# Kernel optimization log

Measured on AMD Instinct MI355X. Metric: run time of the kernel, lower is better.

Reference implementation:

```python
import jax, jax.numpy as jnp
import numpy as np

N_QUBITS = 6
N_LAYERS = 2
DIM = 2 ** N_QUBITS  # 64


def _apply_1q(state, U, q):
    """Apply a 1-qubit gate U on qubit q. state: (B, 2,...,2); U: (2,2) or (B,2,2)."""
    s = jnp.moveaxis(state, 1 + q, -1)
    if U.ndim == 3:  # batched gate (angle embedding)
        s = jnp.einsum('bij,b...j->b...i', U, s)
    else:
        s = jnp.einsum('ij,...j->...i', U, s)
    return jnp.moveaxis(s, -1, 1 + q)


def _cnot(state, c, t):
    """CNOT with control qubit c, target qubit t on (B, 2,...,2) state."""
    ax_c = 1 + c
    s0 = jax.lax.index_in_dim(state, 0, ax_c, keepdims=False)
    s1 = jax.lax.index_in_dim(state, 1, ax_c, keepdims=False)
    ax_t = 1 + t if t < c else t  # target axis index after removing control axis
    s1 = jnp.flip(s1, axis=ax_t)  # X on target where control=1
    return jnp.stack([s0, s1], axis=ax_c)


def _rot(phi, theta, omega):
    """PennyLane Rot(phi,theta,omega) = RZ(omega) RY(theta) RZ(phi), as a (2,2) complex matrix."""
    ct = jnp.cos(theta / 2)
    st = jnp.sin(theta / 2)
    ep = jnp.exp(-0.5j * (phi + omega))
    em = jnp.exp(0.5j * (phi - omega))
    row0 = jnp.stack([ep * ct, -em * st])
    row1 = jnp.stack([jnp.conj(em) * st, jnp.conj(ep) * ct])
    return jnp.stack([row0, row1]).astype(jnp.complex64)


def _circuit(angles, weights):
    """AngleEmbedding (RX) + StronglyEntanglingLayers + per-qubit <Z>. angles: (B, 6)."""
    B = angles.shape[0]
    state = jnp.zeros((B,) + (2,) * N_QUBITS, jnp.complex64)
    state = state.at[(slice(None),) + (0,) * N_QUBITS].set(1.0)

    # AngleEmbedding: RX(angle_q) on each qubit (batched gates)
    for q in range(N_QUBITS):
        half = angles[:, q] / 2
        ct = jnp.cos(half).astype(jnp.complex64)
        st = jnp.sin(half)
        U = jnp.stack([jnp.stack([ct, -1j * st], -1),
                       jnp.stack([-1j * st, ct], -1)], -2)  # (B,2,2)
        state = _apply_1q(state, U, q)

    # StronglyEntanglingLayers: per-layer Rot on each qubit, then CNOT ring with range r
    for l in range(N_LAYERS):
        for q in range(N_QUBITS):
            state = _apply_1q(state, _rot(weights[l, q, 0], weights[l, q, 1], weights[l, q, 2]), q)
        r = (l % (N_QUBITS - 1)) + 1
        for q in range(N_QUBITS):
            state = _cnot(state, q, (q + r) % N_QUBITS)

    probs = (state.real ** 2 + state.imag ** 2).reshape(B, DIM)  # (B, 64)
    # <Z_q> = sum_i probs[i] * (1 - 2*bit_q(i)); qubit 0 is the most-significant axis
    bits = (jnp.arange(DIM)[None, :] >> (N_QUBITS - 1 - jnp.arange(N_QUBITS))[:, None]) & 1
    signs = (1 - 2 * bits).astype(probs.dtype)  # (6, 64)
    return probs @ signs.T  # (B, 6)


def setup_inputs() -> dict:
    key = jax.random.key(0)
    k1, k2, k3, k4 = jax.random.split(key, 4)
    B, D = 65536, 512
    x = jax.random.normal(k1, (B, D), jnp.float32)
    W = jax.random.normal(k2, (N_QUBITS, D), jnp.float32) / np.float32(np.sqrt(D))
    b = jax.random.normal(k3, (N_QUBITS,), jnp.float32) * 0.01
    weights = jax.random.uniform(k4, (N_LAYERS, N_QUBITS, 3), jnp.float32, 0.0, 2 * np.pi)
    return {"x": x, "W": W, "b": b, "weights": weights}


def reference(x, W, b, weights):
    z = x @ W.T + b                                   # (B, 6)
    z = z / jnp.linalg.norm(z, axis=1, keepdims=True)  # L2 normalize per row
    return _circuit(z, weights)                        # (B, 6) Pauli-Z expvals
```

## Files before the change

kernel.cpp:

```cpp
#include <hip/hip_runtime.h>
#include <math.h>

#define NQ 6
#define NLAYERS 2
#define ROW_D 512

typedef short short8 __attribute__((ext_vector_type(8)));
typedef float f32x4 __attribute__((ext_vector_type(4)));

__device__ __forceinline__ ushort f2bf(float f) {
    unsigned u = __float_as_uint(f);
    return (ushort)((u + 0x7fffu + ((u >> 16) & 1u)) >> 16);
}
__device__ __forceinline__ float bf2f(ushort h) {
    return __uint_as_float((unsigned)h << 16);
}
__device__ __forceinline__ float merge_red(float u, float v, int m, int lane) {
    float send = (lane & m) ? u : v;
    float recv = __shfl_xor(send, m, 64);
    return ((lane & m) ? v : u) + recv;
}

__global__ __launch_bounds__(256) void gen_tables(
    const float* __restrict__ weights, const float* __restrict__ W,
    ushort* __restrict__ ws)
{
    const int tid = threadIdx.x;

    {
        const int base = (blockIdx.x * 256 + tid) * 2;
        #pragma unroll
        for (int e = 0; e < 2; ++e) {
            const int i = base + e;
            const int n = i >> 9, k = i & 511;
            ushort v = 0;
            if (n < NQ) {
                v = f2bf(W[(n << 9) | k]);
            } else if (n >= 8 && n < 8 + NQ) {
                const float w = W[((n - 8) << 9) | k];
                v = f2bf(w - bf2f(f2bf(w)));
            }
            ws[8192 + i] = v;
        }
    }

    __shared__ __align__(16) float gmat[NLAYERS * NQ * 8];
    if (tid < NLAYERS * NQ) {
        float phi = weights[tid * 3 + 0];
        float th  = weights[tid * 3 + 1];
        float om  = weights[tid * 3 + 2];
        float st, ct, sA, cA, sB, cB;
        __sincosf(0.5f * th, &st, &ct);
        __sincosf(0.5f * (phi + om), &sA, &cA);
        __sincosf(0.5f * (phi - om), &sB, &cB);
        float* g = &gmat[tid * 8];
        g[0] =  cA * ct;  g[1] = -sA * ct;
        g[2] = -cB * st;  g[3] = -sB * st;
        g[4] =  cA * ct;  g[5] =  sA * ct;
        g[6] =  cB * st;  g[7] = -sB * st;
    }
    __syncthreads();

    const int lane = tid & 63;
    const int wave = tid >> 6;
    const int jj = blockIdx.x * 4 + wave;

    int srcA = lane;
    #pragma unroll
    for (int q = NQ - 1; q >= 0; --q) {
        const int t = (q + 1) % NQ;
        srcA ^= ((srcA >> (5 - q)) & 1) << (5 - t);
    }
    int srcB = lane;
    #pragma unroll
    for (int q = NQ - 1; q >= 0; --q) {
        const int t = (q + 2) % NQ;
        srcB ^= ((srcB >> (5 - q)) & 1) << (5 - t);
    }
    const int adA = srcA << 2, adB = srcB << 2;

    float sr = (lane == jj) ? 1.f : 0.f;
    float si = 0.f;
    #pragma unroll
    for (int l = 0; l < NLAYERS; ++l) {
        #pragma unroll
        for (int q = 0; q < NQ; ++q) {
            const int bp = 5 - q, m = 1 << bp;
            const int bit = (lane >> bp) & 1;
            const float4 g = *reinterpret_cast<const float4*>(
                &gmat[((l * NQ + q) << 3) + (bit << 2)]);
            float pr = __shfl_xor(sr, m, 64);
            float pi = __shfl_xor(si, m, 64);
            float nr = g.x * sr - g.y * si + g.z * pr - g.w * pi;
            float ni = g.x * si + g.y * sr + g.z * pi + g.w * pr;
            sr = nr; si = ni;
        }
        const int ad = (l == 0) ? adA : adB;
        sr = __int_as_float(__builtin_amdgcn_ds_bpermute(ad, __float_as_int(sr)));
        si = __int_as_float(__builtin_amdgcn_ds_bpermute(ad, __float_as_int(si)));
    }

    const int pc = __popc(jj) & 3;
    float r2, i2;
    if      (pc == 1) { r2 =  si; i2 = -sr; }
    else if (pc == 2) { r2 = -sr; i2 = -si; }
    else if (pc == 3) { r2 = -si; i2 =  sr; }
    else              { r2 =  sr; i2 =  si; }
    ws[lane * 64 + jj]        = f2bf(r2);
    ws[4096 + lane * 64 + jj] = f2bf(i2);
}

__global__ __launch_bounds__(256, 4) void qmain(
    const float* __restrict__ x, const float* __restrict__ bvec,
    const ushort* __restrict__ ws, float* __restrict__ out, int B)
{
    __shared__ short8 Mlds[2][64][8];
    __shared__ short8 Wlds[16][64];
    __shared__ float2 trans[4][144];
    const int tid = threadIdx.x;

    const short8* mg = reinterpret_cast<const short8*>(ws);
    #pragma unroll
    for (int i = 0; i < 4; ++i) {
        const int idx = tid + i * 256;
        short8 v = mg[idx];
        const int mat = idx >> 9, row = (idx >> 3) & 63, c = idx & 7;
        Mlds[mat][row][c ^ (row & 7)] = v;
    }
    #pragma unroll
    for (int i = 0; i < 4; ++i) {
        const int idx = tid + i * 256;
        short8 v = mg[1024 + idx];
        const int n = idx >> 6, c = idx & 63;
        Wlds[n][c ^ (n & 7)] = v;
    }
    __syncthreads();

    const int lane = tid & 63;
    const int wave = tid >> 6;
    const int g  = lane >> 4;
    const int l4 = lane & 15;
    const int swz = l4 & 7;
    const int rowbase = blockIdx.x * 64 + wave * 16;

    f32x4 zacc = {0.f, 0.f, 0.f, 0.f};
    const float* xrow = x + (size_t)(rowbase + l4) * ROW_D + g * 8;
    #pragma unroll 8
    for (int kt = 0; kt < 16; ++kt) {
        const float4 xa = *reinterpret_cast<const float4*>(xrow + kt * 32);
        const float4 xb = *reinterpret_cast<const float4*>(xrow + kt * 32 + 4);
        short8 af;
        af[0] = (short)f2bf(xa.x); af[1] = (short)f2bf(xa.y);
        af[2] = (short)f2bf(xa.z); af[3] = (short)f2bf(xa.w);
        af[4] = (short)f2bf(xb.x); af[5] = (short)f2bf(xb.y);
        af[6] = (short)f2bf(xb.z); af[7] = (short)f2bf(xb.w);
        const short8 bw = Wlds[l4][(kt * 4 + g) ^ swz];
        zacc = __builtin_amdgcn_mfma_f32_16x16x32_bf16(af, bw, zacc, 0, 0, 0);
    }

    const float bn = (l4 < NQ) ? bvec[l4] : 0.f;
    #pragma unroll
    for (int reg = 0; reg < 4; ++reg) {
        const float zlo = __shfl_xor(zacc[reg], 8, 64);
        const float zv = zacc[reg] + zlo + bn;
        float s2 = (l4 < NQ) ? zv * zv : 0.f;
        s2 += __shfl_xor(s2, 1, 64);
        s2 += __shfl_xor(s2, 2, 64);
        s2 += __shfl_xor(s2, 4, 64);
        s2 += __shfl_xor(s2, 8, 64);
        const float ang = 0.5f * zv * rsqrtf(s2);
        float sv, cv;
        __sincosf(ang, &sv, &cv);
        if (l4 < NQ)
            trans[wave][(g * 4 + reg) * 9 + l4] = make_float2(cv, sv);
    }

    float cq[NQ], sq[NQ];
    #pragma unroll
    for (int q = 0; q < NQ; ++q) {
        const float2 cs = trans[wave][l4 * 9 + q];
        cq[q] = cs.x; sq[q] = cs.y;
    }
    float m45[4];
    m45[0] = cq[4] * cq[5]; m45[1] = cq[4] * sq[5];
    m45[2] = sq[4] * cq[5]; m45[3] = sq[4] * sq[5];
    float pl[8];
    #pragma unroll
    for (int j = 0; j < 8; ++j)
        pl[j] = ((j & 4) ? sq[3] : cq[3]) * m45[j & 3];
    const float t12 = ((g & 2) ? sq[1] : cq[1]) * ((g & 1) ? sq[2] : cq[2]);
    const float ph0 = cq[0] * t12;
    const float ph1 = sq[0] * t12;
    short8 a0, a1;
    #pragma unroll
    for (int j = 0; j < 8; ++j) {
        a0[j] = (short)f2bf(ph0 * pl[j]);
        a1[j] = (short)f2bf(ph1 * pl[j]);
    }

    f32x4 cre[4] = {}, cim[4] = {};
    #pragma unroll
    for (int nt = 0; nt < 4; ++nt) {
        const int brow = nt * 16 + l4;
        const short8 br0 = Mlds[0][brow][(g)     ^ swz];
        const short8 br1 = Mlds[0][brow][(4 + g) ^ swz];
        const short8 bi0 = Mlds[1][brow][(g)     ^ swz];
        const short8 bi1 = Mlds[1][brow][(4 + g) ^ swz];
        cre[nt] = __builtin_amdgcn_mfma_f32_16x16x32_bf16(a0, br0, cre[nt], 0, 0, 0);
        cre[nt] = __builtin_amdgcn_mfma_f32_16x16x32_bf16(a1, br1, cre[nt], 0, 0, 0);
        cim[nt] = __builtin_amdgcn_mfma_f32_16x16x32_bf16(a0, bi0, cim[nt], 0, 0, 0);
        cim[nt] = __builtin_amdgcn_mfma_f32_16x16x32_bf16(a1, bi1, cim[nt], 0, 0, 0);
    }

    const int col = l4;
    #pragma unroll
    for (int reg = 0; reg < 4; ++reg) {
        const float p0 = cre[0][reg] * cre[0][reg] + cim[0][reg] * cim[0][reg];
        const float p1 = cre[1][reg] * cre[1][reg] + cim[1][reg] * cim[1][reg];
        const float p2 = cre[2][reg] * cre[2][reg] + cim[2][reg] * cim[2][reg];
        const float p3 = cre[3][reg] * cre[3][reg] + cim[3][reg] * cim[3][reg];
        float t  = (p0 + p1) + (p2 + p3);
        float y0 = (p0 + p1) - (p2 + p3);
        float y1 = (p0 + p2) - (p1 + p3);
        #pragma unroll
        for (int m = 1; m <= 8; m <<= 1) {
            float rcv = __shfl_xor(t, m, 64);
            t = (lane & m) ? (rcv - t) : (t + rcv);
        }
        float y = merge_red(y0, y1, 1, lane);
        y += __shfl_xor(y, 2, 64);
        y += __shfl_xor(y, 4, 64);
        y += __shfl_xor(y, 8, 64);
        const size_t orow = (size_t)(rowbase + g * 4 + reg) * 6;
        if      (col == 0) { out[orow + 0] = y; }
        else if (col == 1) { out[orow + 1] = y; out[orow + 5] = t; }
        else if (col == 2) { out[orow + 4] = t; }
        else if (col == 4) { out[orow + 3] = t; }
        else if (col == 8) { out[orow + 2] = t; }
    }
}

extern "C" void kernel_launch(void* const* d_in, const int* in_sizes, int n_in,
                              void* d_out, int out_size, void* d_ws, size_t ws_size,
                              hipStream_t stream) {
    const float* x  = (const float*)d_in[0];
    const float* W  = (const float*)d_in[1];
    const float* bv = (const float*)d_in[2];
    const float* wt = (const float*)d_in[3];
    float* out = (float*)d_out;
    ushort* ws = (ushort*)d_ws;
    const int B = in_sizes[0] / ROW_D;
    gen_tables<<<16, 256, 0, stream>>>(wt, W, ws);
    qmain<<<B / 64, 256, 0, stream>>>(x, bv, ws, out, B);
}
```

Baseline: 37.52 us.

## Stream x rows through LDS with async global_load_lds ring buffer

Replaces direct per-lane float4 global loads of x with asynchronous global_load_lds into a four-slot per-wave LDS ring. Each iteration waits on vmcnt, reads the staged slice, then issues the next two loads, so memory traffic overlaps with the MFMA work. The circuit matrices are now read directly from global memory (likely L2-resident) instead of being copied into LDS, which frees shared memory and drops a staging pass. The hand-placed waitcnt and sched_barrier ordering is fragile, and the global matrix reads add latency to the tail of the kernel.

```diff
diff --git a/kernel.cpp b/kernel.cpp
--- a/kernel.cpp
+++ b/kernel.cpp
@@ -19,6 +19,11 @@
     float send = (lane & m) ? u : v;
     float recv = __shfl_xor(send, m, 64);
     return ((lane & m) ? v : u) + recv;
+}
+__device__ __forceinline__ void gload16(const float* g, void* ldsbase) {
+    __builtin_amdgcn_global_load_lds(
+        (const __attribute__((address_space(1))) void*)g,
+        (__attribute__((address_space(3))) void*)ldsbase, 16, 0, 0);
 }
 
 __global__ __launch_bounds__(256) void gen_tables(
@@ -26,7 +31,6 @@
     ushort* __restrict__ ws)
 {
     const int tid = threadIdx.x;
-
     {
         const int base = (blockIdx.x * 256 + tid) * 2;
         #pragma unroll
@@ -114,19 +118,12 @@
     const float* __restrict__ x, const float* __restrict__ bvec,
     const ushort* __restrict__ ws, float* __restrict__ out, int B)
 {
-    __shared__ short8 Mlds[2][64][8];
     __shared__ short8 Wlds[16][64];
+    __shared__ float4 xstage[4][4][64];
     __shared__ float2 trans[4][144];
     const int tid = threadIdx.x;
 
     const short8* mg = reinterpret_cast<const short8*>(ws);
-    #pragma unroll
-    for (int i = 0; i < 4; ++i) {
-        const int idx = tid + i * 256;
-        short8 v = mg[idx];
-        const int mat = idx >> 9, row = (idx >> 3) & 63, c = idx & 7;
-        Mlds[mat][row][c ^ (row & 7)] = v;
-    }
     #pragma unroll
     for (int i = 0; i < 4; ++i) {
         const int idx = tid + i * 256;
@@ -143,12 +140,26 @@
     const int swz = l4 & 7;
     const int rowbase = blockIdx.x * 64 + wave * 16;
 
+    const float bn = (l4 < NQ) ? bvec[l4] : 0.f;
+    asm volatile("s_waitcnt vmcnt(0)" ::: "memory");
+    __builtin_amdgcn_sched_barrier(0);
+
+    const float* gbase = x + (size_t)(rowbase + l4) * ROW_D + (lane >> 4) * 4;
+
+    #pragma unroll
+    for (int h = 0; h < 4; ++h)
+        gload16(gbase + h * 16, &xstage[wave][h][0]);
+
     f32x4 zacc = {0.f, 0.f, 0.f, 0.f};
-    const float* xrow = x + (size_t)(rowbase + l4) * ROW_D + g * 8;
-    #pragma unroll 8
+    #pragma unroll
     for (int kt = 0; kt < 16; ++kt) {
-        const float4 xa = *reinterpret_cast<const float4*>(xrow + kt * 32);
-        const float4 xb = *reinterpret_cast<const float4*>(xrow + kt * 32 + 4);
+        if (kt < 15) { asm volatile("s_waitcnt vmcnt(2)" ::: "memory"); }
+        else         { asm volatile("s_waitcnt vmcnt(0)" ::: "memory"); }
+        __builtin_amdgcn_sched_barrier(0);
+
+        const int slot = (2 * kt + (g >> 1)) & 3;
+        const float4 xa = xstage[wave][slot][(g & 1) * 32 + l4];
+        const float4 xb = xstage[wave][slot][(g & 1) * 32 + 16 + l4];
         short8 af;
         af[0] = (short)f2bf(xa.x); af[1] = (short)f2bf(xa.y);
         af[2] = (short)f2bf(xa.z); af[3] = (short)f2bf(xa.w);
@@ -156,9 +167,16 @@
         af[6] = (short)f2bf(xb.z); af[7] = (short)f2bf(xb.w);
         const short8 bw = Wlds[l4][(kt * 4 + g) ^ swz];
         zacc = __builtin_amdgcn_mfma_f32_16x16x32_bf16(af, bw, zacc, 0, 0, 0);
-    }
-
-    const float bn = (l4 < NQ) ? bvec[l4] : 0.f;
+
+        if (kt < 14) {
+            asm volatile("s_waitcnt lgkmcnt(0)" ::: "memory");
+            __builtin_amdgcn_sched_barrier(0);
+            gload16(gbase + (2 * kt + 4) * 16, &xstage[wave][(2 * kt + 4) & 3][0]);
+            gload16(gbase + (2 * kt + 5) * 16, &xstage[wave][(2 * kt + 5) & 3][0]);
+            __builtin_amdgcn_sched_barrier(0);
+        }
+    }
+
     #pragma unroll
     for (int reg = 0; reg < 4; ++reg) {
         const float zlo = __shfl_xor(zacc[reg], 8, 64);
@@ -202,10 +220,10 @@
     #pragma unroll
     for (int nt = 0; nt < 4; ++nt) {
         const int brow = nt * 16 + l4;
-        const short8 br0 = Mlds[0][brow][(g)     ^ swz];
-        const short8 br1 = Mlds[0][brow][(4 + g) ^ swz];
-        const short8 bi0 = Mlds[1][brow][(g)     ^ swz];
-        const short8 bi1 = Mlds[1][brow][(4 + g) ^ swz];
+        const short8 br0 = mg[brow * 8 + g];
+        const short8 br1 = mg[brow * 8 + 4 + g];
+        const short8 bi0 = mg[512 + brow * 8 + g];
+        const short8 bi1 = mg[512 + brow * 8 + 4 + g];
         cre[nt] = __builtin_amdgcn_mfma_f32_16x16x32_bf16(a0, br0, cre[nt], 0, 0, 0);
         cre[nt] = __builtin_amdgcn_mfma_f32_16x16x32_bf16(a1, br1, cre[nt], 0, 0, 0);
         cim[nt] = __builtin_amdgcn_mfma_f32_16x16x32_bf16(a0, bi0, cim[nt], 0, 0, 0);
```

After: 42.06 us. 12.1% more time.

## Split fused kernel into separate GEMV and quantum-tail kernels

Applied to the files above, without the earlier changes.

Splits the single fused kernel into two launches: a bf16 MFMA GEMV that writes the raw projection accumulators to workspace, and a tail kernel that reads them back, normalizes, builds the state and applies the circuit matrices loaded straight from global memory instead of LDS. The aim is to shrink each kernel's LDS and register footprint and the LDS staging of the circuit matrices, which may raise occupancy in the memory-bound GEMV. In exchange it adds an extra kernel launch and a round trip of the intermediate z through global memory, and the tail now reads B operands from global or cache rather than LDS.

```diff
diff --git a/kernel.cpp b/kernel.cpp
--- a/kernel.cpp
+++ b/kernel.cpp
@@ -26,7 +26,6 @@
     ushort* __restrict__ ws)
 {
     const int tid = threadIdx.x;
-
     {
         const int base = (blockIdx.x * 256 + tid) * 2;
         #pragma unroll
@@ -110,23 +109,13 @@
     ws[4096 + lane * 64 + jj] = f2bf(i2);
 }
 
-__global__ __launch_bounds__(256, 4) void qmain(
-    const float* __restrict__ x, const float* __restrict__ bvec,
-    const ushort* __restrict__ ws, float* __restrict__ out, int B)
+__global__ __launch_bounds__(256, 4) void zgemv(
+    const float* __restrict__ x, const ushort* __restrict__ ws,
+    float4* __restrict__ zout, int B)
 {
-    __shared__ short8 Mlds[2][64][8];
     __shared__ short8 Wlds[16][64];
-    __shared__ float2 trans[4][144];
     const int tid = threadIdx.x;
-
     const short8* mg = reinterpret_cast<const short8*>(ws);
-    #pragma unroll
-    for (int i = 0; i < 4; ++i) {
-        const int idx = tid + i * 256;
-        short8 v = mg[idx];
-        const int mat = idx >> 9, row = (idx >> 3) & 63, c = idx & 7;
-        Mlds[mat][row][c ^ (row & 7)] = v;
-    }
     #pragma unroll
     for (int i = 0; i < 4; ++i) {
         const int idx = tid + i * 256;
@@ -141,10 +130,11 @@
     const int g  = lane >> 4;
     const int l4 = lane & 15;
     const int swz = l4 & 7;
-    const int rowbase = blockIdx.x * 64 + wave * 16;
+
+    const int chunk = blockIdx.x * 4 + wave;
+    const float* xrow = x + (size_t)chunk * 16 * ROW_D + (size_t)l4 * ROW_D + g * 8;
 
     f32x4 zacc = {0.f, 0.f, 0.f, 0.f};
-    const float* xrow = x + (size_t)(rowbase + l4) * ROW_D + g * 8;
     #pragma unroll 8
     for (int kt = 0; kt < 16; ++kt) {
         const float4 xa = *reinterpret_cast<const float4*>(xrow + kt * 32);
@@ -157,6 +147,25 @@
         const short8 bw = Wlds[l4][(kt * 4 + g) ^ swz];
         zacc = __builtin_amdgcn_mfma_f32_16x16x32_bf16(af, bw, zacc, 0, 0, 0);
     }
+    zout[(size_t)chunk * 64 + lane] = *reinterpret_cast<float4*>(&zacc);
+}
+
+__global__ __launch_bounds__(256, 4) void qtail(
+    const float4* __restrict__ zin, const float* __restrict__ bvec,
+    const ushort* __restrict__ ws, float* __restrict__ out, int B)
+{
+    __shared__ float2 trans[4][144];
+    const int tid = threadIdx.x;
+    const int lane = tid & 63;
+    const int wave = tid >> 6;
+    const int g  = lane >> 4;
+    const int l4 = lane & 15;
+    const short8* mg = reinterpret_cast<const short8*>(ws);
+
+    const int chunk = blockIdx.x * 4 + wave;
+    const int rowbase = chunk * 16;
+    const float4 zt = zin[(size_t)chunk * 64 + lane];
+    const f32x4 zacc = {zt.x, zt.y, zt.z, zt.w};
 
     const float bn = (l4 < NQ) ? bvec[l4] : 0.f;
     #pragma unroll
@@ -202,10 +211,10 @@
     #pragma unroll
     for (int nt = 0; nt < 4; ++nt) {
         const int brow = nt * 16 + l4;
-        const short8 br0 = Mlds[0][brow][(g)     ^ swz];
-        const short8 br1 = Mlds[0][brow][(4 + g) ^ swz];
-        const short8 bi0 = Mlds[1][brow][(g)     ^ swz];
-        const short8 bi1 = Mlds[1][brow][(4 + g) ^ swz];
+        const short8 br0 = mg[brow * 8 + g];
+        const short8 br1 = mg[brow * 8 + 4 + g];
+        const short8 bi0 = mg[512 + brow * 8 + g];
+        const short8 bi1 = mg[512 + brow * 8 + 4 + g];
         cre[nt] = __builtin_amdgcn_mfma_f32_16x16x32_bf16(a0, br0, cre[nt], 0, 0, 0);
         cre[nt] = __builtin_amdgcn_mfma_f32_16x16x32_bf16(a1, br1, cre[nt], 0, 0, 0);
         cim[nt] = __builtin_amdgcn_mfma_f32_16x16x32_bf16(a0, bi0, cim[nt], 0, 0, 0);
@@ -249,7 +258,10 @@
     const float* wt = (const float*)d_in[3];
     float* out = (float*)d_out;
     ushort* ws = (ushort*)d_ws;
+    float4* zt = (float4*)((char*)d_ws + 32768);
     const int B = in_sizes[0] / ROW_D;
+    const int chunks = B / 16;
     gen_tables<<<16, 256, 0, stream>>>(wt, W, ws);
-    qmain<<<B / 64, 256, 0, stream>>>(x, bv, ws, out, B);
-}
+    zgemv<<<chunks / 4, 256, 0, stream>>>(x, ws, zt, B);
+    qtail<<<chunks / 4, 256, 0, stream>>>(zt, bv, ws, out, B);
+}
```

Result: slower. 44.37 us (+18.2%).
